# Optimization experiments

Hardware: AMD Instinct MI355X
Metric: run time of the kernel (lower is better)

## Reference

```python
import jax, jax.numpy as jnp
import numpy as np

B, N, D, H, DEPTH, MLP_DIM = 8, 1024, 256, 8, 4, 1024
INNER = D * H  # quirk of this repo: inner_dim = dim * n_heads
LN_EPS = 1e-3  # keras LayerNormalization default epsilon


def setup_inputs() -> dict:
    key = jax.random.key(0)
    ks = jax.random.split(key, 6)
    def nrm(k, shape, s=0.02):
        return jax.random.normal(k, shape, dtype=jnp.float32) * s
    return {
        "x": jax.random.normal(ks[0], (B, N, D), dtype=jnp.float32),
        # PreNorm LayerNorm(axis=1): params have shape (N,) per layer
        "ln1_g": jnp.ones((DEPTH, N), jnp.float32),
        "ln1_b": jnp.zeros((DEPTH, N), jnp.float32),
        "w_qkv": nrm(ks[1], (DEPTH, D, 3 * INNER)),
        "w_out": nrm(ks[2], (DEPTH, INNER, D)),
        "b_out": jnp.zeros((DEPTH, D), jnp.float32),
        "ln2_g": jnp.ones((DEPTH, N), jnp.float32),
        "ln2_b": jnp.zeros((DEPTH, N), jnp.float32),
        "w1": nrm(ks[3], (DEPTH, D, MLP_DIM)),
        "b1": jnp.zeros((DEPTH, MLP_DIM), jnp.float32),
        "w2": nrm(ks[4], (DEPTH, MLP_DIM, D)),
        "b2": jnp.zeros((DEPTH, D), jnp.float32),
    }


def _ln_axis1(x, g, b):
    # keras LayerNormalization(axis=1): normalize over sequence axis
    mu = jnp.mean(x, axis=1, keepdims=True)
    var = jnp.var(x, axis=1, keepdims=True)
    return (x - mu) * jax.lax.rsqrt(var + LN_EPS) * g[None, :, None] + b[None, :, None]


def _split_heads(t):
    # b n (h d) -> b h n d, with per-head dim d == D
    return t.reshape(B, N, H, D).transpose(0, 2, 1, 3)


def reference(x, ln1_g, ln1_b, w_qkv, w_out, b_out, ln2_g, ln2_b, w1, b1, w2, b2):
    scale = D ** -0.5
    for i in range(DEPTH):
        # --- PreNorm + MHA ---
        h = _ln_axis1(x, ln1_g[i], ln1_b[i])
        qkv = h @ w_qkv[i]                               # [B,N,3*INNER]
        q, k, v = jnp.split(qkv, 3, axis=-1)
        q, k, v = _split_heads(q), _split_heads(k), _split_heads(v)
        dot = jnp.einsum('bhid,bhjd->bhij', q, k) * scale  # [B,H,N,N]
        A = jax.nn.softmax(dot, axis=-1)
        z = jnp.einsum('bhij,bhjd->bhid', A, v)
        z = z.transpose(0, 2, 1, 3).reshape(B, N, INNER)
        x = x + z @ w_out[i] + b_out[i]
        # --- PreNorm + MLP (exact erf GELU) ---
        h = _ln_axis1(x, ln2_g[i], ln2_b[i])
        h = jax.nn.gelu(h @ w1[i] + b1[i], approximate=False)
        x = x + h @ w2[i] + b2[i]
    return x
```

## Files before the change

### kernel.cpp

```cpp
#include <hip/hip_runtime.h>
#include <hip/hip_bf16.h>

#define SEQ    1024
#define DM     256
#define NH     8
#define NB     8
#define NLAYER 4
#define MLPD   1024
#define ROWS   (NB*SEQ)
#define QKVW   6144
#define INNERW 2048

typedef __attribute__((ext_vector_type(8))) short bh8;
typedef __attribute__((ext_vector_type(4))) short bh4;
typedef __attribute__((ext_vector_type(4))) float fx4;

__device__ __forceinline__ short f2bf(float f) {
  return __builtin_bit_cast(short, __float2bfloat16(f));
}
__device__ __forceinline__ fx4 mfma16(bh8 a, bh8 b, fx4 c) {
  return __builtin_amdgcn_mfma_f32_16x16x32_bf16(a, b, c, 0, 0, 0);
}
__device__ __forceinline__ void g2l16(const void* g, void* l) {
  __builtin_amdgcn_global_load_lds(
      (const __attribute__((address_space(1))) void*)g,
      (__attribute__((address_space(3))) void*)l, 16, 0, 0);
}
__device__ __forceinline__ int kperm(int r) {
  return ((r & 1) << 2) | ((r >> 1) & 3);
}

__global__ void wtrans_k(const float* __restrict__ src, __hip_bfloat16* __restrict__ dst,
                         int R, int C, size_t sls, size_t dls) {
  src += (size_t)blockIdx.z * sls;
  dst += (size_t)blockIdx.z * dls;
  __shared__ float t[32][33];
  int tx = threadIdx.x, ty = threadIdx.y;
  int r0 = blockIdx.y * 32, c0 = blockIdx.x * 32;
#pragma unroll
  for (int i = 0; i < 32; i += 8) t[ty + i][tx] = src[(size_t)(r0 + ty + i) * C + c0 + tx];
  __syncthreads();
#pragma unroll
  for (int i = 0; i < 32; i += 8)
    dst[(size_t)(c0 + ty + i) * R + r0 + tx] = __float2bfloat16(t[tx][ty + i]);
}

__global__ void ln_k(const float* __restrict__ xf, const float* __restrict__ gam,
                     const float* __restrict__ bet, __hip_bfloat16* __restrict__ h) {
  int b = blockIdx.y, d0 = blockIdx.x * 16;
  int dl = threadIdx.x & 3;
  int nt = threadIdx.x >> 2;
  const float* xb = xf + (size_t)b * SEQ * DM + d0 + dl * 4;
  fx4 s = 0.f, ss = 0.f;
  for (int n = nt; n < SEQ; n += 64) {
    fx4 v = *(const fx4*)(xb + (size_t)n * DM);
    s += v; ss += v * v;
  }
  __shared__ fx4 S1[64][4], S2[64][4];
  __shared__ fx4 MU[4], RS[4];
  S1[nt][dl] = s; S2[nt][dl] = ss;
  __syncthreads();
  if (nt == 0) {
    fx4 a = 0.f, c = 0.f;
#pragma unroll
    for (int i = 0; i < 64; i++) { a += S1[i][dl]; c += S2[i][dl]; }
    fx4 mu, rs;
#pragma unroll
    for (int r = 0; r < 4; r++) {
      mu[r] = a[r] * (1.f / SEQ);
      float var = c[r] * (1.f / SEQ) - mu[r] * mu[r];
      rs[r] = rsqrtf(var + 1e-3f);
    }
    MU[dl] = mu; RS[dl] = rs;
  }
  __syncthreads();
  fx4 mu = MU[dl], rs = RS[dl];
  __hip_bfloat16* hb = h + (size_t)b * SEQ * DM + d0 + dl * 4;
  for (int n = nt; n < SEQ; n += 64) {
    fx4 v = *(const fx4*)(xb + (size_t)n * DM);
    float gn = gam[n], bn = bet[n];
    bh4 o;
#pragma unroll
    for (int r = 0; r < 4; r++) o[r] = f2bf((v[r] - mu[r]) * rs[r] * gn + bn);
    *(bh4*)(hb + (size_t)n * DM) = o;
  }
}

template <int BM, int BN, int EPI>
__global__ __launch_bounds__(256) void gemm_bt(
    const __hip_bfloat16* __restrict__ A, const __hip_bfloat16* __restrict__ Bt,
    __hip_bfloat16* __restrict__ Cout, const float* __restrict__ bias,
    const float* __restrict__ rin, float* __restrict__ rout,
    __hip_bfloat16* __restrict__ vT, int M, int Nc, int K) {
  constexpr int BK = 64;
  constexpr int NR = BN / 32;
  constexpr int MR = BM / 32;
  static_assert(BN == 64 || BN == 128, "");
  static_assert(BM == 64 || BM == 128, "");
  constexpr int LDSE = (EPI == 3) ? 128 * 132 : (BM + BN) * BK;
  __shared__ __hip_bfloat16 smem[LDSE];
  __hip_bfloat16* As = smem;
  __hip_bfloat16* Bs = smem + BM * BK;
  const int tid = threadIdx.x;
  const int lane = tid & 63, w = tid >> 6;
  const int g = lane >> 4, qr = lane & 15;
  const int wr = w >> 1, wc = w & 1;
  const unsigned aid = blockIdx.y * gridDim.x + blockIdx.x;
  const unsigned nwg = gridDim.x * gridDim.y;
  const unsigned lid = (aid & 7u) * (nwg >> 3) + (aid >> 3);
  const int m0 = (int)(lid / gridDim.x) * BM, n0 = (int)(lid % gridDim.x) * BN;
  const int swr = kperm(qr & 7);

  fx4 acc[MR][NR];
#pragma unroll
  for (int m = 0; m < MR; m++)
#pragma unroll
    for (int n = 0; n < NR; n++) acc[m][n] = 0.f;

  constexpr int ACH = (BM * BK) / (8 * 256);
  constexpr int BCH = (BN * BK) / (8 * 256);

  for (int k0 = 0; k0 < K; k0 += BK) {
    __syncthreads();
#pragma unroll
    for (int c = 0; c < ACH; c++) {
      int idx = tid + c * 256;
      int row = idx >> 3, gr2 = idx & 7;
      g2l16(A + (size_t)(m0 + row) * K + k0 + ((gr2 ^ kperm(row & 7)) << 3), (char*)As + idx * 16);
    }
#pragma unroll
    for (int c = 0; c < BCH; c++) {
      int idx = tid + c * 256;
      int col = idx >> 3, gr2 = idx & 7;
      g2l16(Bt + (size_t)(n0 + col) * K + k0 + ((gr2 ^ kperm(col & 7)) << 3), (char*)Bs + idx * 16);
    }
    __syncthreads();
#pragma unroll
    for (int ks = 0; ks < 2; ks++) {
      bh8 af[MR], bf[NR];
#pragma unroll
      for (int m = 0; m < MR; m++)
        af[m] = *(const bh8*)(As + (wr * (BM / 2) + m * 16 + qr) * BK + (((ks * 4 + g) ^ swr) << 3));
#pragma unroll
      for (int n = 0; n < NR; n++)
        bf[n] = *(const bh8*)(Bs + (wc * (BN / 2) + n * 16 + qr) * BK + (((ks * 4 + g) ^ swr) << 3));
#pragma unroll
      for (int m = 0; m < MR; m++)
#pragma unroll
        for (int n = 0; n < NR; n++) acc[m][n] = mfma16(af[m], bf[n], acc[m][n]);
    }
  }

  if constexpr (EPI == 2) {
#pragma unroll
    for (int n = 0; n < NR; n++) {
      int gc = n0 + wc * (BN / 2) + n * 16 + qr;
      float bv = bias[gc];
#pragma unroll
      for (int m = 0; m < MR; m++) {
        int grb = m0 + wr * (BM / 2) + m * 16 + g * 4;
#pragma unroll
        for (int r = 0; r < 4; r++)
          rout[(size_t)(grb + r) * Nc + gc] = rin[(size_t)(grb + r) * Nc + gc] + acc[m][n][r] + bv;
      }
    }
  } else if (EPI == 3 && n0 >= 4096) {
    __syncthreads();
    __hip_bfloat16* Cs = smem;
#pragma unroll
    for (int n = 0; n < NR; n++) {
      int dl = wc * (BN / 2) + n * 16 + qr;
#pragma unroll
      for (int m = 0; m < MR; m++) {
        int nlp = wr * (BM / 2) + (m >> 1) * 32 + g * 8 + (m & 1) * 4;
        bh4 v;
#pragma unroll
        for (int r = 0; r < 4; r++) v[r] = f2bf(acc[m][n][r]);
        *(bh4*)(Cs + dl * 132 + nlp) = v;
      }
    }
    __syncthreads();
    const int dl = tid >> 1, half = tid & 1;
    const int bb = m0 >> 10;
    const int hh = (n0 - 4096) >> 8;
    const int d0v = (n0 - 4096) & 255;
    __hip_bfloat16* dst =
        vT + ((size_t)(bb * 8 + hh) * 256 + d0v + dl) * SEQ + (m0 & 1023) + half * 64;
#pragma unroll
    for (int j = 0; j < 8; j++)
      *(bh8*)(dst + j * 8) = *(const bh8*)(Cs + dl * 132 + half * 64 + j * 8);
  } else {
#pragma unroll
    for (int n = 0; n < NR; n++) {
      int gc = n0 + wc * (BN / 2) + n * 16 + qr;
      float bv = (EPI == 1) ? bias[gc] : 0.f;
#pragma unroll
      for (int m = 0; m < MR; m++) {
        int grb = m0 + wr * (BM / 2) + m * 16 + g * 4;
#pragma unroll
        for (int r = 0; r < 4; r++) {
          float v = acc[m][n][r];
          if (EPI == 1) {
            v += bv;
            v = 0.5f * v * (1.f + erff(v * 0.70710678118654752f));
          }
          Cout[(size_t)(grb + r) * Nc + gc] = __float2bfloat16(v);
        }
      }
    }
  }
}

__global__ __launch_bounds__(256) void attn_k(
    const __hip_bfloat16* __restrict__ qkv, const __hip_bfloat16* __restrict__ vT,
    __hip_bfloat16* __restrict__ z) {
  __shared__ __hip_bfloat16 Ks[32 * 256];
  __shared__ __hip_bfloat16 Vs[256 * 32];
  const int tid = threadIdx.x;
  const int lane = tid & 63, w = tid >> 6;
  const int g = lane >> 4, qr = lane & 15;
  const unsigned aid = (blockIdx.z * NH + blockIdx.y) * (SEQ / 64) + blockIdx.x;
  const unsigned lid = (aid & 7u) * 128u + (aid >> 3);
  const int qi = lid & 15, hh = (lid >> 4) & 7, b = lid >> 7;
  const int q0 = qi * 64 + w * 16;
  const size_t qkv_b = (size_t)b * SEQ * QKVW;

  bh8 qf[8];
  {
    const __hip_bfloat16* qrow = qkv + qkv_b + (size_t)(q0 + qr) * QKVW + hh * 256 + g * 8;
#pragma unroll
    for (int kd = 0; kd < 8; kd++) qf[kd] = *(const bh8*)(qrow + kd * 32);
  }

  fx4 o[16];
#pragma unroll
  for (int i = 0; i < 16; i++) o[i] = 0.f;
  float m_run = -INFINITY, l_run = 0.f;
  constexpr float cL = 0.0625f * 1.44269504f;

  const int ksw = kperm(qr & 7);
  const int vsw = ((qr >> 1) & 3);

  for (int j0 = 0; j0 < SEQ; j0 += 32) {
    __syncthreads();
#pragma unroll
    for (int c = 0; c < 4; c++) {
      int idx = tid + c * 256;
      int key = idx >> 5, c16 = idx & 31;
      int dp = (c16 ^ kperm(key & 7)) << 3;
      g2l16(qkv + qkv_b + (size_t)(j0 + key) * QKVW + 2048 + hh * 256 + dp, (char*)Ks + idx * 16);
    }
    const __hip_bfloat16* vb = vT + ((size_t)(b * 8 + hh) * 256) * SEQ + j0;
#pragma unroll
    for (int c = 0; c < 4; c++) {
      int idx = tid + c * 256;
      int d = idx >> 2, gr = idx & 3;
      int np = (gr ^ ((d >> 1) & 3)) << 3;
      g2l16(vb + (size_t)d * SEQ + np, (char*)Vs + idx * 16);
    }
    __syncthreads();

    fx4 s0 = 0.f, s1 = 0.f;
#pragma unroll
    for (int kd = 0; kd < 8; kd++) {
      bh8 k0f = *(const bh8*)(Ks + (size_t)qr * 256 + (((kd * 4 + g) ^ ksw) << 3));
      bh8 k1f = *(const bh8*)(Ks + (size_t)(16 + qr) * 256 + (((kd * 4 + g) ^ ksw) << 3));
      s0 = mfma16(k0f, qf[kd], s0);
      s1 = mfma16(k1f, qf[kd], s1);
    }
    float sv[8];
#pragma unroll
    for (int r = 0; r < 4; r++) { sv[r] = s0[r]; sv[4 + r] = s1[r]; }
    float pmax = sv[0];
#pragma unroll
    for (int i = 1; i < 8; i++) pmax = fmaxf(pmax, sv[i]);
    pmax = fmaxf(pmax, __shfl_xor(pmax, 16));
    pmax = fmaxf(pmax, __shfl_xor(pmax, 32));
    if (!__all(pmax <= m_run + 128.f)) {
      float m_new = fmaxf(m_run, pmax);
      float corr = __builtin_amdgcn_exp2f((m_run - m_new) * cL);
#pragma unroll
      for (int nd = 0; nd < 16; nd++) {
        o[nd][0] *= corr; o[nd][1] *= corr; o[nd][2] *= corr; o[nd][3] *= corr;
      }
      l_run *= corr;
      m_run = m_new;
    }
    float mL = m_run * cL;
    float p[8], ps = 0.f;
#pragma unroll
    for (int i = 0; i < 8; i++) {
      p[i] = __builtin_amdgcn_exp2f(fmaf(sv[i], cL, -mL));
      ps += p[i];
    }
    ps += __shfl_xor(ps, 16);
    ps += __shfl_xor(ps, 32);
    l_run += ps;
    bh8 pa;
#pragma unroll
    for (int i = 0; i < 8; i++) pa[i] = f2bf(p[i]);
#pragma unroll
    for (int nd = 0; nd < 16; nd++) {
      int d = nd * 16 + qr;
      bh8 vf = *(const bh8*)(Vs + (size_t)d * 32 + ((g ^ vsw) << 3));
      o[nd] = mfma16(vf, pa, o[nd]);
    }
  }

  float inv = 1.f / l_run;
  __hip_bfloat16* zb = z + (size_t)b * SEQ * INNERW + hh * 256 + (size_t)(q0 + qr) * INNERW;
#pragma unroll
  for (int nd = 0; nd < 16; nd++) {
    bh4 ov;
#pragma unroll
    for (int r = 0; r < 4; r++) ov[r] = f2bf(o[nd][r] * inv);
    *(bh4*)(zb + nd * 16 + g * 4) = ov;
  }
}

extern "C" void kernel_launch(void* const* d_in, const int* in_sizes, int n_in,
                              void* d_out, int out_size, void* d_ws, size_t ws_size,
                              hipStream_t stream) {
  const float* x_in  = (const float*)d_in[0];
  const float* ln1g  = (const float*)d_in[1];
  const float* ln1b  = (const float*)d_in[2];
  const float* w_qkv = (const float*)d_in[3];
  const float* w_out = (const float*)d_in[4];
  const float* b_out = (const float*)d_in[5];
  const float* ln2g  = (const float*)d_in[6];
  const float* ln2b  = (const float*)d_in[7];
  const float* w1    = (const float*)d_in[8];
  const float* b1    = (const float*)d_in[9];
  const float* w2    = (const float*)d_in[10];
  const float* b2    = (const float*)d_in[11];

  char* ws = (char*)d_ws;
  size_t off = 0;
  auto alloc = [&](size_t bytes) { char* p = ws + off; off += (bytes + 255) & ~(size_t)255; return p; };
  float*          xf    = (float*)         alloc((size_t)ROWS * DM * 4);
  __hip_bfloat16* h     = (__hip_bfloat16*)alloc((size_t)ROWS * DM * 2);
  __hip_bfloat16* qkv   = (__hip_bfloat16*)alloc((size_t)ROWS * QKVW * 2);
  __hip_bfloat16* vT    = (__hip_bfloat16*)alloc((size_t)NB * NH * 256 * SEQ * 2);
  __hip_bfloat16* zbuf  = (__hip_bfloat16*)alloc((size_t)ROWS * INNERW * 2);
  __hip_bfloat16* mh    = zbuf;
  __hip_bfloat16* wqkvT = (__hip_bfloat16*)alloc((size_t)NLAYER * QKVW * DM * 2);
  __hip_bfloat16* woutT = (__hip_bfloat16*)alloc((size_t)NLAYER * DM * INNERW * 2);
  __hip_bfloat16* w1T   = (__hip_bfloat16*)alloc((size_t)NLAYER * MLPD * DM * 2);
  __hip_bfloat16* w2T   = (__hip_bfloat16*)alloc((size_t)NLAYER * DM * MLPD * 2);
  (void)ws_size; (void)in_sizes; (void)n_in; (void)out_size;

  wtrans_k<<<dim3(QKVW / 32, DM / 32, NLAYER), dim3(32, 8), 0, stream>>>(
      w_qkv, wqkvT, DM, QKVW, (size_t)DM * QKVW, (size_t)DM * QKVW);
  wtrans_k<<<dim3(DM / 32, INNERW / 32, NLAYER), dim3(32, 8), 0, stream>>>(
      w_out, woutT, INNERW, DM, (size_t)INNERW * DM, (size_t)INNERW * DM);
  wtrans_k<<<dim3(MLPD / 32, DM / 32, NLAYER), dim3(32, 8), 0, stream>>>(
      w1, w1T, DM, MLPD, (size_t)DM * MLPD, (size_t)DM * MLPD);
  wtrans_k<<<dim3(DM / 32, MLPD / 32, NLAYER), dim3(32, 8), 0, stream>>>(
      w2, w2T, MLPD, DM, (size_t)MLPD * DM, (size_t)MLPD * DM);

  for (int i = 0; i < NLAYER; i++) {
    const float* xcur = (i == 0) ? x_in : xf;
    float* xnext_out = (i == NLAYER - 1) ? (float*)d_out : xf;

    ln_k<<<dim3(DM / 16, NB), 256, 0, stream>>>(xcur, ln1g + i * SEQ, ln1b + i * SEQ, h);
    gemm_bt<128, 128, 3><<<dim3(QKVW / 128, ROWS / 128), 256, 0, stream>>>(
        h, wqkvT + (size_t)i * QKVW * DM, qkv, nullptr, nullptr, nullptr, vT, ROWS, QKVW, DM);
    attn_k<<<dim3(SEQ / 64, NH, NB), 256, 0, stream>>>(qkv, vT, zbuf);
    gemm_bt<64, 64, 2><<<dim3(DM / 64, ROWS / 64), 256, 0, stream>>>(
        zbuf, woutT + (size_t)i * DM * INNERW, nullptr, b_out + i * DM, xcur, xf, nullptr,
        ROWS, DM, INNERW);
    ln_k<<<dim3(DM / 16, NB), 256, 0, stream>>>(xf, ln2g + i * SEQ, ln2b + i * SEQ, h);
    gemm_bt<128, 128, 1><<<dim3(MLPD / 128, ROWS / 128), 256, 0, stream>>>(
        h, w1T + (size_t)i * MLPD * DM, mh, b1 + i * MLPD, nullptr, nullptr, nullptr,
        ROWS, MLPD, DM);
    gemm_bt<64, 64, 2><<<dim3(DM / 64, ROWS / 64), 256, 0, stream>>>(
        mh, w2T + (size_t)i * DM * MLPD, nullptr, b2 + i * DM, xf, xnext_out, nullptr,
        ROWS, DM, MLPD);
  }
}
```

Measured before the change: 979.7 us.

## Double-buffer GEMM LDS staging, widen LayerNorm grid, retile MLP up-projection

Adds a DBUF template option to the bf16 GEMM. It prefetches the next K tile into a second LDS buffer while the current one is being computed, which removes one barrier per iteration. This is enabled for the out-projection, W1 and W2 GEMMs. W1 is also retiled to 64x128 to launch more workgroups, and the LayerNorm kernel now handles 8 columns per block with a two-level reduction, doubling its block count. The cost is twice the LDS use in those GEMMs and possible occupancy loss; correctness also relies on the async global_load_lds writes being complete by the single barrier at the end of each iteration.

```diff
diff --git a/kernel.cpp b/kernel.cpp
--- a/kernel.cpp
+++ b/kernel.cpp
@@ -47,23 +47,30 @@
 
 __global__ void ln_k(const float* __restrict__ xf, const float* __restrict__ gam,
                      const float* __restrict__ bet, __hip_bfloat16* __restrict__ h) {
-  int b = blockIdx.y, d0 = blockIdx.x * 16;
-  int dl = threadIdx.x & 3;
-  int nt = threadIdx.x >> 2;
+  int b = blockIdx.y, d0 = blockIdx.x * 8;
+  int dl = threadIdx.x & 1;
+  int nt = threadIdx.x >> 1;
   const float* xb = xf + (size_t)b * SEQ * DM + d0 + dl * 4;
   fx4 s = 0.f, ss = 0.f;
-  for (int n = nt; n < SEQ; n += 64) {
+  for (int n = nt; n < SEQ; n += 128) {
     fx4 v = *(const fx4*)(xb + (size_t)n * DM);
     s += v; ss += v * v;
   }
-  __shared__ fx4 S1[64][4], S2[64][4];
-  __shared__ fx4 MU[4], RS[4];
+  __shared__ fx4 S1[128][2], S2[128][2];
+  __shared__ fx4 MU[2], RS[2];
   S1[nt][dl] = s; S2[nt][dl] = ss;
+  __syncthreads();
+  if (nt < 16) {
+    fx4 a = S1[nt][dl], c = S2[nt][dl];
+#pragma unroll
+    for (int i = 0; i < 7; i++) { a += S1[nt + 16 + i * 16][dl]; c += S2[nt + 16 + i * 16][dl]; }
+    S1[nt][dl] = a; S2[nt][dl] = c;
+  }
   __syncthreads();
   if (nt == 0) {
     fx4 a = 0.f, c = 0.f;
 #pragma unroll
-    for (int i = 0; i < 64; i++) { a += S1[i][dl]; c += S2[i][dl]; }
+    for (int i = 0; i < 16; i++) { a += S1[i][dl]; c += S2[i][dl]; }
     fx4 mu, rs;
 #pragma unroll
     for (int r = 0; r < 4; r++) {
@@ -76,7 +83,7 @@
   __syncthreads();
   fx4 mu = MU[dl], rs = RS[dl];
   __hip_bfloat16* hb = h + (size_t)b * SEQ * DM + d0 + dl * 4;
-  for (int n = nt; n < SEQ; n += 64) {
+  for (int n = nt; n < SEQ; n += 128) {
     fx4 v = *(const fx4*)(xb + (size_t)n * DM);
     float gn = gam[n], bn = bet[n];
     bh4 o;
@@ -86,7 +93,7 @@
   }
 }
 
-template <int BM, int BN, int EPI>
+template <int BM, int BN, int EPI, int DBUF>
 __global__ __launch_bounds__(256) void gemm_bt(
     const __hip_bfloat16* __restrict__ A, const __hip_bfloat16* __restrict__ Bt,
     __hip_bfloat16* __restrict__ Cout, const float* __restrict__ bias,
@@ -95,12 +102,11 @@
   constexpr int BK = 64;
   constexpr int NR = BN / 32;
   constexpr int MR = BM / 32;
+  constexpr int SPAN = (BM + BN) * BK;
   static_assert(BN == 64 || BN == 128, "");
   static_assert(BM == 64 || BM == 128, "");
-  constexpr int LDSE = (EPI == 3) ? 128 * 132 : (BM + BN) * BK;
+  constexpr int LDSE = (EPI == 3) ? 128 * 132 : SPAN * (DBUF ? 2 : 1);
   __shared__ __hip_bfloat16 smem[LDSE];
-  __hip_bfloat16* As = smem;
-  __hip_bfloat16* Bs = smem + BM * BK;
   const int tid = threadIdx.x;
   const int lane = tid & 63, w = tid >> 6;
   const int g = lane >> 4, qr = lane & 15;
@@ -120,34 +126,55 @@
   constexpr int ACH = (BM * BK) / (8 * 256);
   constexpr int BCH = (BN * BK) / (8 * 256);
 
-  for (int k0 = 0; k0 < K; k0 += BK) {
-    __syncthreads();
+  auto stage = [&](int buf, int k0) {
+    __hip_bfloat16* As_ = smem + buf * SPAN;
+    __hip_bfloat16* Bs_ = As_ + BM * BK;
 #pragma unroll
     for (int c = 0; c < ACH; c++) {
       int idx = tid + c * 256;
       int row = idx >> 3, gr2 = idx & 7;
-      g2l16(A + (size_t)(m0 + row) * K + k0 + ((gr2 ^ kperm(row & 7)) << 3), (char*)As + idx * 16);
+      g2l16(A + (size_t)(m0 + row) * K + k0 + ((gr2 ^ kperm(row & 7)) << 3), (char*)As_ + idx * 16);
     }
 #pragma unroll
     for (int c = 0; c < BCH; c++) {
       int idx = tid + c * 256;
       int col = idx >> 3, gr2 = idx & 7;
-      g2l16(Bt + (size_t)(n0 + col) * K + k0 + ((gr2 ^ kperm(col & 7)) << 3), (char*)Bs + idx * 16);
-    }
-    __syncthreads();
+      g2l16(Bt + (size_t)(n0 + col) * K + k0 + ((gr2 ^ kperm(col & 7)) << 3), (char*)Bs_ + idx * 16);
+    }
+  };
+  auto comp = [&](const __hip_bfloat16* As_, const __hip_bfloat16* Bs_) {
 #pragma unroll
     for (int ks = 0; ks < 2; ks++) {
       bh8 af[MR], bf[NR];
 #pragma unroll
       for (int m = 0; m < MR; m++)
-        af[m] = *(const bh8*)(As + (wr * (BM / 2) + m * 16 + qr) * BK + (((ks * 4 + g) ^ swr) << 3));
+        af[m] = *(const bh8*)(As_ + (wr * (BM / 2) + m * 16 + qr) * BK + (((ks * 4 + g) ^ swr) << 3));
 #pragma unroll
       for (int n = 0; n < NR; n++)
-        bf[n] = *(const bh8*)(Bs + (wc * (BN / 2) + n * 16 + qr) * BK + (((ks * 4 + g) ^ swr) << 3));
+        bf[n] = *(const bh8*)(Bs_ + (wc * (BN / 2) + n * 16 + qr) * BK + (((ks * 4 + g) ^ swr) << 3));
 #pragma unroll
       for (int m = 0; m < MR; m++)
 #pragma unroll
         for (int n = 0; n < NR; n++) acc[m][n] = mfma16(af[m], bf[n], acc[m][n]);
+    }
+  };
+
+  if constexpr (DBUF) {
+    stage(0, 0);
+    __syncthreads();
+    const int NT = K / BK;
+    for (int t = 0; t < NT; ++t) {
+      const int cur = t & 1;
+      if (t + 1 < NT) stage(cur ^ 1, (t + 1) * BK);
+      comp(smem + cur * SPAN, smem + cur * SPAN + BM * BK);
+      __syncthreads();
+    }
+  } else {
+    for (int k0 = 0; k0 < K; k0 += BK) {
+      __syncthreads();
+      stage(0, k0);
+      __syncthreads();
+      comp(smem, smem + BM * BK);
     }
   }
 
@@ -362,18 +389,18 @@
     const float* xcur = (i == 0) ? x_in : xf;
     float* xnext_out = (i == NLAYER - 1) ? (float*)d_out : xf;
 
-    ln_k<<<dim3(DM / 16, NB), 256, 0, stream>>>(xcur, ln1g + i * SEQ, ln1b + i * SEQ, h);
-    gemm_bt<128, 128, 3><<<dim3(QKVW / 128, ROWS / 128), 256, 0, stream>>>(
+    ln_k<<<dim3(DM / 8, NB), 256, 0, stream>>>(xcur, ln1g + i * SEQ, ln1b + i * SEQ, h);
+    gemm_bt<128, 128, 3, 0><<<dim3(QKVW / 128, ROWS / 128), 256, 0, stream>>>(
         h, wqkvT + (size_t)i * QKVW * DM, qkv, nullptr, nullptr, nullptr, vT, ROWS, QKVW, DM);
     attn_k<<<dim3(SEQ / 64, NH, NB), 256, 0, stream>>>(qkv, vT, zbuf);
-    gemm_bt<64, 64, 2><<<dim3(DM / 64, ROWS / 64), 256, 0, stream>>>(
+    gemm_bt<64, 64, 2, 1><<<dim3(DM / 64, ROWS / 64), 256, 0, stream>>>(
         zbuf, woutT + (size_t)i * DM * INNERW, nullptr, b_out + i * DM, xcur, xf, nullptr,
         ROWS, DM, INNERW);
-    ln_k<<<dim3(DM / 16, NB), 256, 0, stream>>>(xf, ln2g + i * SEQ, ln2b + i * SEQ, h);
-    gemm_bt<128, 128, 1><<<dim3(MLPD / 128, ROWS / 128), 256, 0, stream>>>(
+    ln_k<<<dim3(DM / 8, NB), 256, 0, stream>>>(xf, ln2g + i * SEQ, ln2b + i * SEQ, h);
+    gemm_bt<64, 128, 1, 1><<<dim3(MLPD / 128, ROWS / 64), 256, 0, stream>>>(
         h, w1T + (size_t)i * MLPD * DM, mh, b1 + i * MLPD, nullptr, nullptr, nullptr,
         ROWS, MLPD, DM);
-    gemm_bt<64, 64, 2><<<dim3(DM / 64, ROWS / 64), 256, 0, stream>>>(
+    gemm_bt<64, 64, 2, 1><<<dim3(DM / 64, ROWS / 64), 256, 0, stream>>>(
         mh, w2T + (size_t)i * DM * MLPD, nullptr, b2 + i * DM, xf, xnext_out, nullptr,
         ROWS, DM, MLPD);
   }
```

After: 961.4 us. About the same (-1.9%).
